# Kernel tuning notes

Hardware: AMD Instinct MI355X
Metric: run time of the kernel (lower is better)

The kernel has to match this reference:

```python
import jax, jax.numpy as jnp
import numpy as np

BLOCKSIZE = 64  # bitsandbytes default blocksize for NF4

# NF4 codebook: 16 normalized-float-4 quantile values (bitsandbytes)
NF4_CODE = jnp.array([
    -1.0, -0.6961928009986877, -0.5250730514526367, -0.39491748809814453,
    -0.28444138169288635, -0.18477343022823334, -0.09105003625154495, 0.0,
    0.07958029955625534, 0.16093020141124725, 0.24611230194568634,
    0.33791524171829224, 0.44070982933044434, 0.5626170039176941,
    0.7229568362236023, 1.0], dtype=jnp.float32)


def setup_inputs() -> dict:
    key = jax.random.key(0)
    k1, k2, k3, k4 = jax.random.split(key, 4)
    B, S, IN, OUT = 2, 512, 4096, 11008
    x = jax.random.normal(k1, (B, S, IN), dtype=jnp.float32)
    # 4-bit NF4 codebook indices (packed storage modeled as unpacked indices)
    w_idx = jax.random.randint(k2, (OUT, IN), 0, 16, dtype=jnp.int32)
    # per-block absmax scales over the flattened weight, blocksize 64
    absmax = jax.random.uniform(k3, (OUT * IN // BLOCKSIZE,), dtype=jnp.float32)
    bias = jax.random.normal(k4, (OUT,), dtype=jnp.float32)
    return {"x": x, "w_idx": w_idx, "absmax": absmax, "bias": bias}


def dequantize_nf4(w_idx, absmax):
    # w_idx: [OUT, IN] int indices into NF4 codebook
    # absmax: [OUT*IN/BLOCKSIZE] per-block scales
    OUT, IN = w_idx.shape
    vals = NF4_CODE[w_idx]  # [OUT, IN]
    scales = absmax.reshape(OUT * IN // BLOCKSIZE, 1)
    w = (vals.reshape(-1, BLOCKSIZE) * scales).reshape(OUT, IN)
    return w


def reference(x, w_idx, absmax, bias):
    # Faithful to forward: dequantize full weight, then F.linear(x, W, b) = x @ W.T + b
    w = dequantize_nf4(w_idx, absmax)          # [OUT, IN]
    out = jnp.einsum('bsi,oi->bso', x, w) + bias  # [B, S, OUT]
    return out
```

## Files before the change

### kernel.cpp

```cpp
#include <hip/hip_runtime.h>
#include <hip/hip_bf16.h>
#include <stdint.h>


using short8 = __attribute__((ext_vector_type(8))) short;
using f32x4  = __attribute__((ext_vector_type(4))) float;

#define AS1 __attribute__((address_space(1)))
#define AS3 __attribute__((address_space(3)))

__device__ __forceinline__ void gload16(const void* g, void* l) {
  __builtin_amdgcn_global_load_lds((const AS1 uint32_t*)g, (AS3 uint32_t*)l, 16, 0, 0);
}

__constant__ float NF4_CONST[16] = {
  -1.0f, -0.6961928009986877f, -0.5250730514526367f, -0.39491748809814453f,
  -0.28444138169288635f, -0.18477343022823334f, -0.09105003625154495f, 0.0f,
  0.07958029955625534f, 0.16093020141124725f, 0.24611230194568634f,
  0.33791524171829224f, 0.44070982933044434f, 0.5626170039176941f,
  0.7229568362236023f, 1.0f};

__device__ __forceinline__ ushort f2bf(float f) {
  union { float f; uint32_t u; } v; v.f = f;
  uint32_t r = (v.u + 0x7FFFu + ((v.u >> 16) & 1u)) >> 16;
  return (ushort)r;
}

__global__ __launch_bounds__(256) void f32_to_bf16(
    const float* __restrict__ in, ushort* __restrict__ out) {
  const int t = blockIdx.x * 256 + threadIdx.x;
  const int base = t * 8;
  const float4 a = *(const float4*)(in + base);
  const float4 b = *(const float4*)(in + base + 4);
  uint4 o;
  o.x = (uint32_t)f2bf(a.x) | ((uint32_t)f2bf(a.y) << 16);
  o.y = (uint32_t)f2bf(a.z) | ((uint32_t)f2bf(a.w) << 16);
  o.z = (uint32_t)f2bf(b.x) | ((uint32_t)f2bf(b.y) << 16);
  o.w = (uint32_t)f2bf(b.z) | ((uint32_t)f2bf(b.w) << 16);
  *(uint4*)(out + base) = o;
}

#define BM 128
#define BN 128
#define BKK 64

#define DQ2(dst, ia, ib, s) do {                                          \
  float _a = lutf[(ia)] * (s);                                            \
  float _b = lutf[(ib)] * (s);                                            \
  dst = (__builtin_bit_cast(uint32_t, _a) >> 16) |                        \
        (__builtin_bit_cast(uint32_t, _b) & 0xffff0000u);                 \
} while (0)

__global__ __launch_bounds__(256, 2) void gemm_fused(
    const ushort* __restrict__ A, const int* __restrict__ widx,
    const float* __restrict__ absmax, const float* __restrict__ bias,
    float* __restrict__ C, const int M, const int N, const int K,
    const int MP, const int NB) {
  __shared__ char lds[32768 + 64];
  float* lutf = (float*)(lds + 32768);
  const int tid  = threadIdx.x;
  const int wid  = tid >> 6;
  const int lane = tid & 63;

  const int r8 = blockIdx.x & 7;
  const int w  = blockIdx.x >> 3;
  const int mP = w % MP;
  const int q  = w / MP;
  const int nP = (q << 3) + r8;
  if (nP >= NB) return;
  const int row0 = mP * BM;
  const int col0 = nP * BN;
  const int wr = wid >> 1, wc = wid & 1;
  const int KB = K >> 6;

  if (tid < 16) lutf[tid] = NF4_CONST[tid];

  const ushort* gsrcA[4];
  const int*    wsrc[4];
  const float*  asrc[4];
  int bdst[4];
#pragma unroll
  for (int i = 0; i < 4; ++i) {
    const int u = tid + i * 256;
    const int rr = u >> 3;
    const int sl = (u & 7) ^ (rr & 7);
    gsrcA[i] = A + (size_t)(row0 + rr) * K + sl * 8;
    wsrc[i]  = widx + (size_t)(col0 + rr) * K + sl * 8;
    asrc[i]  = absmax + (size_t)(col0 + rr) * KB;
    bdst[i]  = 16384 + i * 4096 + tid * 16;
  }

  int offA[2][4], offB[2][4];
#pragma unroll
  for (int ks = 0; ks < 2; ++ks) {
#pragma unroll
    for (int m = 0; m < 4; ++m) {
      const int ra = wr * 64 + m * 16 + (lane & 15);
      offA[ks][m] = ra * 128 + (((ks * 4 + (lane >> 4)) ^ (ra & 7)) * 16);
      const int rb = wc * 64 + m * 16 + (lane & 15);
      offB[ks][m] = 16384 + rb * 128 + (((ks * 4 + (lane >> 4)) ^ (rb & 7)) * 16);
    }
  }

  f32x4 acc[4][4] = {};

  int4 q0[4], q1[4]; float sc[4];
#pragma unroll
  for (int i = 0; i < 4; ++i) {
    q0[i] = *(const int4*)(wsrc[i]);
    q1[i] = *(const int4*)(wsrc[i] + 4);
    sc[i] = asrc[i][0];
  }
  __syncthreads();

  for (int kt = 0; kt < K; kt += BKK) {
#pragma unroll
    for (int i = 0; i < 4; ++i)
      gload16(gsrcA[i] + kt, lds + i * 4096 + wid * 1024);
#pragma unroll
    for (int i = 0; i < 4; ++i) {
      uint4 v;
      DQ2(v.x, q0[i].x, q0[i].y, sc[i]);
      DQ2(v.y, q0[i].z, q0[i].w, sc[i]);
      DQ2(v.z, q1[i].x, q1[i].y, sc[i]);
      DQ2(v.w, q1[i].z, q1[i].w, sc[i]);
      *(uint4*)(lds + bdst[i]) = v;
    }
    __syncthreads();

    if (kt + BKK < K) {
      const int kn = kt + BKK;
#pragma unroll
      for (int i = 0; i < 4; ++i) {
        q0[i] = *(const int4*)(wsrc[i] + kn);
        q1[i] = *(const int4*)(wsrc[i] + kn + 4);
        sc[i] = asrc[i][kn >> 6];
      }
    }

#pragma unroll
    for (int ks = 0; ks < 2; ++ks) {
      short8 af[4], bv[4];
#pragma unroll
      for (int m = 0; m < 4; ++m) af[m] = *(const short8*)(lds + offA[ks][m]);
#pragma unroll
      for (int n = 0; n < 4; ++n) bv[n] = *(const short8*)(lds + offB[ks][n]);
#pragma unroll
      for (int m = 0; m < 4; ++m)
#pragma unroll
        for (int n = 0; n < 4; ++n)
          acc[m][n] = __builtin_amdgcn_mfma_f32_16x16x32_bf16(
              af[m], bv[n], acc[m][n], 0, 0, 0);
    }
    __syncthreads();
  }

#pragma unroll
  for (int n = 0; n < 4; ++n) {
    const int gc = col0 + wc * 64 + n * 16 + (lane & 15);
    const float bvadd = bias[gc];
#pragma unroll
    for (int m = 0; m < 4; ++m) {
      const int gr0 = row0 + wr * 64 + m * 16 + ((lane >> 4) * 4);
#pragma unroll
      for (int j = 0; j < 4; ++j)
        C[(size_t)(gr0 + j) * N + gc] = acc[m][n][j] + bvadd;
    }
  }
}

__global__ __launch_bounds__(256) void fallback_kernel(
    const float* __restrict__ x, const int* __restrict__ widx,
    const float* __restrict__ absmax, const float* __restrict__ bias,
    float* __restrict__ out, const int M, const int N, const int K) {
  __shared__ float w[4096];
  const int o = blockIdx.x;
  for (int k = threadIdx.x; k < K; k += 256) {
    const long long fi = (long long)o * K + k;
    w[k] = NF4_CONST[widx[fi]] * absmax[fi >> 6];
  }
  __syncthreads();
  for (int m = threadIdx.x; m < M; m += 256) {
    float acc = bias[o];
    const float* xr = x + (size_t)m * K;
    for (int k = 0; k < K; ++k) acc += xr[k] * w[k];
    out[(size_t)m * N + o] = acc;
  }
}

extern "C" void kernel_launch(void* const* d_in, const int* in_sizes, int n_in,
                              void* d_out, int out_size, void* d_ws, size_t ws_size,
                              hipStream_t stream) {
  const float* x      = (const float*)d_in[0];
  const int*   widx   = (const int*)d_in[1];
  const float* absmax = (const float*)d_in[2];
  const float* bias   = (const float*)d_in[3];
  float* out = (float*)d_out;

  const int N = in_sizes[3];
  const int K = in_sizes[1] / N;
  const int M = in_sizes[0] / K;
  const long long xElems = (long long)M * K;
  const size_t wsNeed = (size_t)xElems * 2;

  if (ws_size >= wsNeed && (M % BM) == 0 && (N % BN) == 0 &&
      (K % BKK) == 0 && (xElems % 2048) == 0) {
    ushort* Xbf = (ushort*)d_ws;
    f32_to_bf16<<<(int)(xElems / (256 * 8)), 256, 0, stream>>>(x, Xbf);
    const int MP = M / BM;
    const int NB = N / BN;
    const int grid = 8 * MP * ((NB + 7) / 8);
    gemm_fused<<<dim3(grid), 256, 0, stream>>>(Xbf, widx, absmax, bias, out,
                                               M, N, K, MP, NB);
  } else {
    fallback_kernel<<<N, 256, 0, stream>>>(x, widx, absmax, bias, out, M, N, K);
  }
}
```

Baseline: 167.5 us.

## Double-buffer activation tile in LDS and prefetch next K-step before compute

The bf16 activation tile now uses two LDS buffers. The next K-slice is loaded asynchronously into the idle buffer while MFMA runs on the current one, and the NF4 index and scale loads for the next step are issued early. The start-of-step __syncthreads is replaced by an explicit lgkmcnt wait plus s_barrier, with sched_barriers added to fix instruction order. LDS grows to about 48KB and launch bounds ask for 3 blocks per CU, which adds register pressure and relies on the compiler to insert the correct vmcnt waits for the LDS DMA.

After: 155.4 us. 7.2% less time.

```diff
diff --git a/kernel.cpp b/kernel.cpp
--- a/kernel.cpp
+++ b/kernel.cpp
@@ -51,13 +51,13 @@
         (__builtin_bit_cast(uint32_t, _b) & 0xffff0000u);                 \
 } while (0)
 
-__global__ __launch_bounds__(256, 2) void gemm_fused(
+__global__ __launch_bounds__(256, 3) void gemm_fused(
     const ushort* __restrict__ A, const int* __restrict__ widx,
     const float* __restrict__ absmax, const float* __restrict__ bias,
     float* __restrict__ C, const int M, const int N, const int K,
     const int MP, const int NB) {
-  __shared__ char lds[32768 + 64];
-  float* lutf = (float*)(lds + 32768);
+  __shared__ char lds[49216];
+  float* lutf = (float*)(lds + 49152);
   const int tid  = threadIdx.x;
   const int wid  = tid >> 6;
   const int lane = tid & 63;
@@ -87,7 +87,7 @@
     gsrcA[i] = A + (size_t)(row0 + rr) * K + sl * 8;
     wsrc[i]  = widx + (size_t)(col0 + rr) * K + sl * 8;
     asrc[i]  = absmax + (size_t)(col0 + rr) * KB;
-    bdst[i]  = 16384 + i * 4096 + tid * 16;
+    bdst[i]  = 32768 + i * 4096 + tid * 16;
   }
 
   int offA[2][4], offB[2][4];
@@ -98,12 +98,15 @@
       const int ra = wr * 64 + m * 16 + (lane & 15);
       offA[ks][m] = ra * 128 + (((ks * 4 + (lane >> 4)) ^ (ra & 7)) * 16);
       const int rb = wc * 64 + m * 16 + (lane & 15);
-      offB[ks][m] = 16384 + rb * 128 + (((ks * 4 + (lane >> 4)) ^ (rb & 7)) * 16);
+      offB[ks][m] = 32768 + rb * 128 + (((ks * 4 + (lane >> 4)) ^ (rb & 7)) * 16);
     }
   }
 
   f32x4 acc[4][4] = {};
 
+#pragma unroll
+  for (int i = 0; i < 4; ++i)
+    gload16(gsrcA[i], lds + i * 4096 + wid * 1024);
   int4 q0[4], q1[4]; float sc[4];
 #pragma unroll
   for (int i = 0; i < 4; ++i) {
@@ -112,11 +115,15 @@
     sc[i] = asrc[i][0];
   }
   __syncthreads();
+  int cur = 0;
 
   for (int kt = 0; kt < K; kt += BKK) {
+    const int ka = (kt + BKK < K) ? kt + BKK : kt;
 #pragma unroll
     for (int i = 0; i < 4; ++i)
-      gload16(gsrcA[i] + kt, lds + i * 4096 + wid * 1024);
+      gload16(gsrcA[i] + ka, lds + ((cur ^ 1) << 14) + i * 4096 + wid * 1024);
+    __builtin_amdgcn_sched_barrier(0);
+
 #pragma unroll
     for (int i = 0; i < 4; ++i) {
       uint4 v;
@@ -126,25 +133,28 @@
       DQ2(v.w, q1[i].z, q1[i].w, sc[i]);
       *(uint4*)(lds + bdst[i]) = v;
     }
-    __syncthreads();
-
-    if (kt + BKK < K) {
-      const int kn = kt + BKK;
-#pragma unroll
-      for (int i = 0; i < 4; ++i) {
-        q0[i] = *(const int4*)(wsrc[i] + kn);
-        q1[i] = *(const int4*)(wsrc[i] + kn + 4);
-        sc[i] = asrc[i][kn >> 6];
-      }
-    }
-
+#pragma unroll
+    for (int i = 0; i < 4; ++i) {
+      q0[i] = *(const int4*)(wsrc[i] + ka);
+      q1[i] = *(const int4*)(wsrc[i] + ka + 4);
+      sc[i] = asrc[i][ka >> 6];
+    }
+    __builtin_amdgcn_sched_barrier(0);
+
+    asm volatile("s_waitcnt lgkmcnt(0)" ::: "memory");
+    __builtin_amdgcn_s_barrier();
+    __builtin_amdgcn_sched_barrier(0);
+
+    const int abase = cur << 14;
 #pragma unroll
     for (int ks = 0; ks < 2; ++ks) {
       short8 af[4], bv[4];
 #pragma unroll
-      for (int m = 0; m < 4; ++m) af[m] = *(const short8*)(lds + offA[ks][m]);
-#pragma unroll
-      for (int n = 0; n < 4; ++n) bv[n] = *(const short8*)(lds + offB[ks][n]);
+      for (int m = 0; m < 4; ++m)
+        af[m] = *(const short8*)(lds + abase + offA[ks][m]);
+#pragma unroll
+      for (int n = 0; n < 4; ++n)
+        bv[n] = *(const short8*)(lds + offB[ks][n]);
 #pragma unroll
       for (int m = 0; m < 4; ++m)
 #pragma unroll
@@ -152,7 +162,10 @@
           acc[m][n] = __builtin_amdgcn_mfma_f32_16x16x32_bf16(
               af[m], bv[n], acc[m][n], 0, 0, 0);
     }
-    __syncthreads();
+    __builtin_amdgcn_sched_barrier(0);
+
+    __builtin_amdgcn_s_barrier();
+    cur ^= 1;
   }
 
 #pragma unroll
```
